# Performance work log

Measured on AMD Instinct MI355X. Metric: run time of the kernel, lower is better.

Reference implementation:

```python
import jax, jax.numpy as jnp
import numpy as np

DIM = 512
HEADS = 16
WIN = (2, 7, 7)
N = WIN[0] * WIN[1] * WIN[2]  # 98
TABLE = (2 * WIN[0] - 1) * (2 * WIN[1] - 1) * (2 * WIN[2] - 1)  # 507


def _rel_pos_index():
    cd, ch, cw = np.arange(WIN[0]), np.arange(WIN[1]), np.arange(WIN[2])
    coords = np.stack(np.meshgrid(cd, ch, cw, indexing='ij'))  # (3, D, H, W)
    flat = coords.reshape(3, -1)  # (3, N)
    rel = flat[:, :, None] - flat[:, None, :]  # (3, N, N)
    rel = rel.transpose(1, 2, 0).copy()
    rel[:, :, 0] += WIN[0] - 1
    rel[:, :, 1] += WIN[1] - 1
    rel[:, :, 2] += WIN[2] - 1
    rel[:, :, 0] *= (2 * WIN[1] - 1) * (2 * WIN[2] - 1)
    rel[:, :, 1] *= 2 * WIN[2] - 1
    return jnp.asarray(rel.sum(-1), dtype=jnp.int32)  # (N, N)


def setup_inputs() -> dict:
    key = jax.random.key(0)
    ks = jax.random.split(key, 7)
    B_ = 1024
    nW = 64
    return {
        'x': jax.random.normal(ks[0], (B_, N, DIM), dtype=jnp.float32),
        'mask': jnp.zeros((nW, N, N), dtype=jnp.float32),
        'qkv_w': jax.random.normal(ks[1], (3 * DIM, DIM), dtype=jnp.float32) * 0.02,
        'qkv_b': jnp.zeros((3 * DIM,), dtype=jnp.float32),
        'proj_w': jax.random.normal(ks[2], (DIM, DIM), dtype=jnp.float32) * 0.02,
        'proj_b': jnp.zeros((DIM,), dtype=jnp.float32),
        'bias_table': jax.random.normal(ks[3], (TABLE, HEADS), dtype=jnp.float32) * 0.02,
        'rel_pos_index': _rel_pos_index(),
    }


def reference(x, mask, qkv_w, qkv_b, proj_w, proj_b, bias_table, rel_pos_index):
    B_, n, C = x.shape
    hd = C // HEADS
    scale = hd ** -0.5
    # qkv projection: (B_, N, 3C) -> (3, B_, H, N, hd)
    qkv = (x @ qkv_w.T + qkv_b).reshape(B_, n, 3, HEADS, hd).transpose(2, 0, 3, 1, 4)
    q, k, v = qkv[0], qkv[1], qkv[2]
    attn = jnp.einsum('bhnd,bhmd->bhnm', q * scale, k)  # (B_, H, N, N)
    # gathered relative position bias: (N, N, H) -> (H, N, N)
    bias = bias_table[rel_pos_index.reshape(-1)].reshape(n, n, HEADS).transpose(2, 0, 1)
    attn = attn + bias[None]
    nW = mask.shape[0]
    attn = attn.reshape(B_ // nW, nW, HEADS, n, n) + mask[None, :, None]
    attn = jax.nn.softmax(attn.reshape(B_, HEADS, n, n), axis=-1)
    out = jnp.einsum('bhnm,bhmd->bnhd', attn, v).reshape(B_, n, C)
    return out @ proj_w.T + proj_b
```

## Files before the change

kernel.cpp:

```cpp
#include <hip/hip_runtime.h>
#include <hip/hip_bf16.h>
#include <stdint.h>

#define DIMC 512
#define NTOK 98

typedef float f32x4 __attribute__((ext_vector_type(4)));
typedef short bf16x8 __attribute__((ext_vector_type(8)));
typedef short bf16x4 __attribute__((ext_vector_type(4)));

__device__ inline unsigned short f2bf(float f) {
    union { float f; uint32_t u; } v; v.f = f;
    uint32_t r = v.u + 0x7fffu + ((v.u >> 16) & 1u);
    return (unsigned short)(r >> 16);
}

__device__ inline bf16x8 cvt8(float4 a, float4 b) {
    bf16x8 r;
    r[0] = (short)f2bf(a.x); r[1] = (short)f2bf(a.y);
    r[2] = (short)f2bf(a.z); r[3] = (short)f2bf(a.w);
    r[4] = (short)f2bf(b.x); r[5] = (short)f2bf(b.y);
    r[6] = (short)f2bf(b.z); r[7] = (short)f2bf(b.w);
    return r;
}

__device__ __forceinline__ void gload16(const void* g, void* l) {
    __builtin_amdgcn_global_load_lds(
        (const __attribute__((address_space(1))) unsigned int*)g,
        (__attribute__((address_space(3))) unsigned int*)l, 16, 0, 0);
}

#define CFENCE() __asm__ __volatile__("" ::: "memory")
#define BARRIER() do { CFENCE(); __builtin_amdgcn_s_barrier(); CFENCE(); } while (0)

__global__ void k_cvt(const float* __restrict__ src, unsigned short* __restrict__ dst,
                      int n8) {
    int i = blockIdx.x * blockDim.x + threadIdx.x;
    if (i < n8) {
        float4 a = *(const float4*)(src + (size_t)i * 8);
        float4 b = *(const float4*)(src + (size_t)i * 8 + 4);
        *(bf16x8*)(dst + (size_t)i * 8) = cvt8(a, b);
    }
}

__global__ void k_bm(const float* __restrict__ table, const int* __restrict__ idx,
                     const float* __restrict__ mask, float* __restrict__ bm_t) {
    int slice = blockIdx.x;
    int b64 = slice >> 4, h = slice & 15;
    float* dst = bm_t + (size_t)slice * 11200;
    const float* mp = mask + (size_t)b64 * 9604;
    for (int t = threadIdx.x; t < 11200; t += blockDim.x) {
        int c = t / 100, i = t - c * 100;
        float v = -1e9f;
        if (c < NTOK && i < NTOK)
            v = (table[idx[i * NTOK + c] * 16 + h] + mp[i * NTOK + c])
                * 1.4426950408889634f;
        dst[t] = v;
    }
}

__global__ __launch_bounds__(512, 2)
void k_qkv3(const unsigned short* __restrict__ xb, const unsigned short* __restrict__ wb,
            const float* __restrict__ qb, unsigned short* __restrict__ qkvbuf) {
    __shared__ unsigned short As[2][2][128 * 64];
    __shared__ unsigned short Bs[2][2][128 * 64];
    const int tid = threadIdx.x;
    const int wid = tid >> 6, l = tid & 63, g = l >> 4, li = l & 15;
    const int wm = wid >> 2, wn = wid & 3;
    const int id = blockIdx.x;
    const int xcd = id & 7, local = id >> 3;
    const int mt = xcd * 49 + local / 6;
    const int nt = local - (local / 6) * 6;
    const int m0 = mt * 256, n0 = nt * 256;

    const int srow = tid >> 3;
    const int scg  = tid & 7;
    const int sxor = (scg ^ (srow & 7)) * 8;
    const unsigned short* aG[2][2];
    const unsigned short* bG[2][2];
    #pragma unroll
    for (int h = 0; h < 2; ++h) {
        aG[h][0] = xb + (size_t)(m0 + h * 128 + srow) * DIMC + sxor;
        aG[h][1] = xb + (size_t)(m0 + h * 128 + 64 + srow) * DIMC + sxor;
        bG[h][0] = wb + (size_t)(n0 + h * 128 + srow) * DIMC + sxor;
        bG[h][1] = wb + (size_t)(n0 + h * 128 + 64 + srow) * DIMC + sxor;
    }
    const int lb0 = wid * 512;
    const int lb1 = 4096 + wid * 512;

    const int axor0 = ((0 + g) ^ (li & 7)) * 8;
    const int axor1 = ((4 + g) ^ (li & 7)) * 8;
    const int arow = li * 64;
    const int brow = (wn & 1) * 4096 + li * 64;
    const int bh = wn >> 1;

    f32x4 acc[8][4] = {};

#define STAGE(s, kt) do {                                   \
        gload16(aG[0][0] + (kt) * 64, &As[s][0][lb0]);      \
        gload16(aG[0][1] + (kt) * 64, &As[s][0][lb1]);      \
        gload16(aG[1][0] + (kt) * 64, &As[s][1][lb0]);      \
        gload16(aG[1][1] + (kt) * 64, &As[s][1][lb1]);      \
        gload16(bG[0][0] + (kt) * 64, &Bs[s][0][lb0]);      \
        gload16(bG[0][1] + (kt) * 64, &Bs[s][0][lb1]);      \
        gload16(bG[1][0] + (kt) * 64, &Bs[s][1][lb0]);      \
        gload16(bG[1][1] + (kt) * 64, &Bs[s][1][lb1]);      } while (0)

    STAGE(0, 0);
    #pragma unroll
    for (int kt = 0; kt < 8; ++kt) {
        const int s = kt & 1;
        if (kt < 7) {
            STAGE(s ^ 1, kt + 1);
            __asm__ __volatile__("s_waitcnt vmcnt(8)" ::: "memory");
        } else {
            __asm__ __volatile__("s_waitcnt vmcnt(0)" ::: "memory");
        }
        BARRIER();
        bf16x8 bfr[4][2];
        #pragma unroll
        for (int nq = 0; nq < 4; ++nq) {
            bfr[nq][0] = *(const bf16x8*)&Bs[s][bh][brow + nq * 1024 + axor0];
            bfr[nq][1] = *(const bf16x8*)&Bs[s][bh][brow + nq * 1024 + axor1];
        }
        #pragma unroll
        for (int q = 0; q < 4; ++q) {
            bf16x8 a00 = *(const bf16x8*)&As[s][wm][arow + (2 * q) * 1024 + axor0];
            bf16x8 a01 = *(const bf16x8*)&As[s][wm][arow + (2 * q) * 1024 + axor1];
            bf16x8 a10 = *(const bf16x8*)&As[s][wm][arow + (2 * q + 1) * 1024 + axor0];
            bf16x8 a11 = *(const bf16x8*)&As[s][wm][arow + (2 * q + 1) * 1024 + axor1];
            __builtin_amdgcn_s_setprio(1);
            #pragma unroll
            for (int nq = 0; nq < 4; ++nq) {
                acc[2 * q][nq] = __builtin_amdgcn_mfma_f32_16x16x32_bf16(
                    bfr[nq][0], a00, acc[2 * q][nq], 0, 0, 0);
                acc[2 * q][nq] = __builtin_amdgcn_mfma_f32_16x16x32_bf16(
                    bfr[nq][1], a01, acc[2 * q][nq], 0, 0, 0);
                acc[2 * q + 1][nq] = __builtin_amdgcn_mfma_f32_16x16x32_bf16(
                    bfr[nq][0], a10, acc[2 * q + 1][nq], 0, 0, 0);
                acc[2 * q + 1][nq] = __builtin_amdgcn_mfma_f32_16x16x32_bf16(
                    bfr[nq][1], a11, acc[2 * q + 1][nq], 0, 0, 0);
            }
            __builtin_amdgcn_s_setprio(0);
        }
        BARRIER();
    }
#undef STAGE

    #pragma unroll
    for (int mq = 0; mq < 8; ++mq) {
        int row = m0 + wm * 128 + mq * 16 + li;
        unsigned bw = (unsigned)row / 98u;
        unsigned nn_ = (unsigned)row - bw * 98u;
        unsigned short* rbase = qkvbuf + (size_t)bw * 150528u + nn_ * 32u;
        #pragma unroll
        for (int nq = 0; nq < 4; ++nq) {
            int col0 = n0 + wn * 64 + nq * 16 + g * 4;
            int which = col0 >> 9;
            int h = (col0 >> 5) & 15;
            int d0 = col0 & 31;
            float4 bv = *(const float4*)(qb + col0);
            float sc = (which == 0)
                ? (0.17677669529663689f * 1.4426950408889634f) : 1.0f;
            bf16x4 pk;
            pk[0] = (short)f2bf((acc[mq][nq][0] + bv.x) * sc);
            pk[1] = (short)f2bf((acc[mq][nq][1] + bv.y) * sc);
            pk[2] = (short)f2bf((acc[mq][nq][2] + bv.z) * sc);
            pk[3] = (short)f2bf((acc[mq][nq][3] + bv.w) * sc);
            *(bf16x4*)(rbase + (size_t)(h * 3 + which) * 3136u + d0) = pk;
        }
    }
}

__global__ __launch_bounds__(512, 2)
void k_proj3(const unsigned short* __restrict__ qkvbuf,
             const unsigned short* __restrict__ wb,
             const float* __restrict__ pb, float* __restrict__ out) {
    __shared__ unsigned short As[2][2][128 * 64];
    __shared__ unsigned short Bs[2][2][128 * 64];
    const int tid = threadIdx.x;
    const int wid = tid >> 6, l = tid & 63, g = l >> 4, li = l & 15;
    const int wm = wid >> 2, wn = wid & 3;
    const int id = blockIdx.x;
    const int xcd = id & 7, local = id >> 3;
    const int mt = xcd * 49 + local / 2;
    const int nt = local & 1;
    const int m0 = mt * 256, n0 = nt * 256;

    const int srow = tid >> 3;
    const int scg  = tid & 7;
    const int cgx  = scg ^ (srow & 7);
    const unsigned short* aG[2][2];
    const unsigned short* bG[2][2];
    #pragma unroll
    for (int h = 0; h < 2; ++h) {
        #pragma unroll
        for (int i = 0; i < 2; ++i) {
            int R = m0 + h * 128 + i * 64 + srow;
            unsigned bw = (unsigned)R / 98u, nn = (unsigned)R - bw * 98u;
            aG[h][i] = qkvbuf + (size_t)bw * 150528u + nn * 32u
                       + (size_t)(cgx >> 2) * 9408u + (cgx & 3) * 8;
            bG[h][i] = wb + (size_t)(n0 + h * 128 + i * 64 + srow) * DIMC + cgx * 8;
        }
    }
    const int lb0 = wid * 512;
    const int lb1 = 4096 + wid * 512;

    const int axor0 = ((0 + g) ^ (li & 7)) * 8;
    const int axor1 = ((4 + g) ^ (li & 7)) * 8;
    const int arow = li * 64;
    const int brow = (wn & 1) * 4096 + li * 64;
    const int bh = wn >> 1;

    f32x4 acc[8][4] = {};

#define STAGE(s, kt) do {                                               \
        gload16(aG[0][0] + (size_t)(kt) * 18816u, &As[s][0][lb0]);      \
        gload16(aG[0][1] + (size_t)(kt) * 18816u, &As[s][0][lb1]);      \
        gload16(aG[1][0] + (size_t)(kt) * 18816u, &As[s][1][lb0]);      \
        gload16(aG[1][1] + (size_t)(kt) * 18816u, &As[s][1][lb1]);      \
        gload16(bG[0][0] + (kt) * 64, &Bs[s][0][lb0]);                  \
        gload16(bG[0][1] + (kt) * 64, &Bs[s][0][lb1]);                  \
        gload16(bG[1][0] + (kt) * 64, &Bs[s][1][lb0]);                  \
        gload16(bG[1][1] + (kt) * 64, &Bs[s][1][lb1]);                  } while (0)

    STAGE(0, 0);
    #pragma unroll
    for (int kt = 0; kt < 8; ++kt) {
        const int s = kt & 1;
        if (kt < 7) {
            STAGE(s ^ 1, kt + 1);
            __asm__ __volatile__("s_waitcnt vmcnt(8)" ::: "memory");
        } else {
            __asm__ __volatile__("s_waitcnt vmcnt(0)" ::: "memory");
        }
        BARRIER();
        bf16x8 bfr[4][2];
        #pragma unroll
        for (int nq = 0; nq < 4; ++nq) {
            bfr[nq][0] = *(const bf16x8*)&Bs[s][bh][brow + nq * 1024 + axor0];
            bfr[nq][1] = *(const bf16x8*)&Bs[s][bh][brow + nq * 1024 + axor1];
        }
        #pragma unroll
        for (int q = 0; q < 4; ++q) {
            bf16x8 a00 = *(const bf16x8*)&As[s][wm][arow + (2 * q) * 1024 + axor0];
            bf16x8 a01 = *(const bf16x8*)&As[s][wm][arow + (2 * q) * 1024 + axor1];
            bf16x8 a10 = *(const bf16x8*)&As[s][wm][arow + (2 * q + 1) * 1024 + axor0];
            bf16x8 a11 = *(const bf16x8*)&As[s][wm][arow + (2 * q + 1) * 1024 + axor1];
            __builtin_amdgcn_s_setprio(1);
            #pragma unroll
            for (int nq = 0; nq < 4; ++nq) {
                acc[2 * q][nq] = __builtin_amdgcn_mfma_f32_16x16x32_bf16(
                    bfr[nq][0], a00, acc[2 * q][nq], 0, 0, 0);
                acc[2 * q][nq] = __builtin_amdgcn_mfma_f32_16x16x32_bf16(
                    bfr[nq][1], a01, acc[2 * q][nq], 0, 0, 0);
                acc[2 * q + 1][nq] = __builtin_amdgcn_mfma_f32_16x16x32_bf16(
                    bfr[nq][0], a10, acc[2 * q + 1][nq], 0, 0, 0);
                acc[2 * q + 1][nq] = __builtin_amdgcn_mfma_f32_16x16x32_bf16(
                    bfr[nq][1], a11, acc[2 * q + 1][nq], 0, 0, 0);
            }
            __builtin_amdgcn_s_setprio(0);
        }
        BARRIER();
    }
#undef STAGE

    #pragma unroll
    for (int mq = 0; mq < 8; ++mq) {
        int row2 = m0 + wm * 128 + mq * 16 + li;
        float* orow = out + (size_t)row2 * DIMC;
        #pragma unroll
        for (int nq = 0; nq < 4; ++nq) {
            int col0 = n0 + wn * 64 + nq * 16 + g * 4;
            float4 bv = *(const float4*)(pb + col0);
            float4 v;
            v.x = acc[mq][nq][0] + bv.x;
            v.y = acc[mq][nq][1] + bv.y;
            v.z = acc[mq][nq][2] + bv.z;
            v.w = acc[mq][nq][3] + bv.w;
            *(float4*)(orow + col0) = v;
        }
    }
}

__global__ __launch_bounds__(448)
void k_attn(unsigned short* __restrict__ qkvbuf, const float* __restrict__ bm_t) {
    __shared__ short Ks[112][36];
    __shared__ short Vt[32][132];
    __shared__ short Ps[7][16][132];

    const int tid = threadIdx.x;
    const int w = tid >> 6, l = tid & 63, g = l >> 4, li = l & 15;
    const int bh = blockIdx.x;
    const int slice = bh & 1023;

    unsigned short* qslot = qkvbuf + (size_t)bh * 3 * 3136;
    const unsigned short* kslot = qslot + 3136;
    const unsigned short* vslot = qslot + 6272;

    const float* bmp = bm_t + (size_t)slice * 11200 + (16 * w + g * 4);
    f32x4 bmf[7];
    #pragma unroll
    for (int j = 0; j < 7; ++j)
        bmf[j] = *(const f32x4*)(bmp + (16 * j + li) * 100);

    bf16x8 aq = *(const bf16x8*)(qslot + (16 * w + li) * 32 + g * 8);

    if (tid < 392) {
        int row = tid >> 2, seg = (tid & 3) * 8;
        bf16x8 kv = *(const bf16x8*)(kslot + row * 32 + seg);
        *(bf16x8*)&Ks[row][seg] = kv;
        bf16x8 vv = *(const bf16x8*)(vslot + row * 32 + seg);
        #pragma unroll
        for (int j = 0; j < 8; ++j) Vt[seg + j][row] = vv[j];
    }
    Ks[98 + (tid >> 5)][tid & 31] = 0;
    for (int t2 = tid; t2 < 32 * 34; t2 += 448) {
        int d = t2 / 34, c = t2 % 34;
        Vt[d][98 + c] = 0;
    }
    for (int t2 = l; t2 < 16 * 20; t2 += 64) {
        int r = t2 / 20, c = t2 % 20;
        Ps[w][r][112 + c] = 0;
    }

    __syncthreads();

    f32x4 s[7];
    __builtin_amdgcn_s_setprio(1);
    #pragma unroll
    for (int j = 0; j < 7; ++j) {
        bf16x8 bk = *(bf16x8*)&Ks[16 * j + li][g * 8];
        s[j] = __builtin_amdgcn_mfma_f32_16x16x32_bf16(aq, bk, bmf[j], 0, 0, 0);
    }
    __builtin_amdgcn_s_setprio(0);

    float sinv[4];
    #pragma unroll
    for (int r = 0; r < 4; ++r) {
        float mx = s[0][r];
        #pragma unroll
        for (int j = 1; j < 7; ++j) mx = fmaxf(mx, s[j][r]);
        mx = fmaxf(mx, __shfl_xor(mx, 1));
        mx = fmaxf(mx, __shfl_xor(mx, 2));
        mx = fmaxf(mx, __shfl_xor(mx, 4));
        mx = fmaxf(mx, __shfl_xor(mx, 8));
        float sum = 0.f;
        #pragma unroll
        for (int j = 0; j < 7; ++j) {
            float p = exp2f(s[j][r] - mx);
            sum += p;
            Ps[w][g * 4 + r][16 * j + li] = (short)f2bf(p);
        }
        sum += __shfl_xor(sum, 1);
        sum += __shfl_xor(sum, 2);
        sum += __shfl_xor(sum, 4);
        sum += __shfl_xor(sum, 8);
        sinv[r] = 1.0f / sum;
    }

    __syncthreads();

    f32x4 o[2] = {};
    __builtin_amdgcn_s_setprio(1);
    #pragma unroll
    for (int ks = 0; ks < 4; ++ks) {
        bf16x8 pa = *(bf16x8*)&Ps[w][li][ks * 32 + g * 8];
        #pragma unroll
        for (int ct = 0; ct < 2; ++ct) {
            bf16x8 vb = *(bf16x8*)&Vt[ct * 16 + li][ks * 32 + g * 8];
            o[ct] = __builtin_amdgcn_mfma_f32_16x16x32_bf16(pa, vb, o[ct], 0, 0, 0);
        }
    }
    __builtin_amdgcn_s_setprio(0);

    #pragma unroll
    for (int ct = 0; ct < 2; ++ct) {
        #pragma unroll
        for (int r = 0; r < 4; ++r) {
            int i = 16 * w + g * 4 + r;
            if (i < NTOK) {
                int d = ct * 16 + li;
                qslot[i * 32 + d] = f2bf(o[ct][r] * sinv[r]);
            }
        }
    }
}

__global__ void k_bias(const float* __restrict__ table, const int* __restrict__ idx,
                       float* __restrict__ bias_full) {
    int h = blockIdx.x, i = blockIdx.y, j = threadIdx.x;
    if (j < NTOK)
        bias_full[(h * NTOK + i) * NTOK + j] = table[idx[i * NTOK + j] * 16 + h];
}

__global__ __launch_bounds__(256)
void k_qkv_old(const float* __restrict__ x, const float* __restrict__ w,
               const float* __restrict__ qb, unsigned short* __restrict__ qkvbuf) {
    __shared__ short As[128][36];
    __shared__ short Bs[128][36];
    const int tid = threadIdx.x;
    const int m0 = blockIdx.x * 128, n0 = blockIdx.y * 128;
    const int wid = tid >> 6, l = tid & 63;
    const int wr = wid >> 1, wc = wid & 1;
    const int g = l >> 4, li = l & 15;
    const int srow = tid >> 1, scol = (tid & 1) * 16;

    f32x4 acc[4][4] = {};
    const float* ap = x + (size_t)(m0 + srow) * DIMC + scol;
    const float* bp = w + (size_t)(n0 + srow) * DIMC + scol;

    for (int k0 = 0; k0 < DIMC; k0 += 32) {
        float4 a0 = *(const float4*)(ap + k0);
        float4 a1 = *(const float4*)(ap + k0 + 4);
        float4 a2 = *(const float4*)(ap + k0 + 8);
        float4 a3 = *(const float4*)(ap + k0 + 12);
        float4 b0 = *(const float4*)(bp + k0);
        float4 b1 = *(const float4*)(bp + k0 + 4);
        float4 b2 = *(const float4*)(bp + k0 + 8);
        float4 b3 = *(const float4*)(bp + k0 + 12);
        *(bf16x8*)&As[srow][scol]     = cvt8(a0, a1);
        *(bf16x8*)&As[srow][scol + 8] = cvt8(a2, a3);
        *(bf16x8*)&Bs[srow][scol]     = cvt8(b0, b1);
        *(bf16x8*)&Bs[srow][scol + 8] = cvt8(b2, b3);
        __syncthreads();
        bf16x8 af[4], bfr[4];
        #pragma unroll
        for (int mm = 0; mm < 4; ++mm)
            af[mm] = *(bf16x8*)&As[wr * 64 + mm * 16 + li][g * 8];
        #pragma unroll
        for (int nn = 0; nn < 4; ++nn)
            bfr[nn] = *(bf16x8*)&Bs[wc * 64 + nn * 16 + li][g * 8];
        #pragma unroll
        for (int mm = 0; mm < 4; ++mm)
            #pragma unroll
            for (int nn = 0; nn < 4; ++nn)
                acc[mm][nn] = __builtin_amdgcn_mfma_f32_16x16x32_bf16(
                    af[mm], bfr[nn], acc[mm][nn], 0, 0, 0);
        __syncthreads();
    }

    #pragma unroll
    for (int mm = 0; mm < 4; ++mm) {
        #pragma unroll
        for (int nn = 0; nn < 4; ++nn) {
            int col = n0 + wc * 64 + nn * 16 + li;
            int which = col >> 9;
            int h = (col >> 5) & 15;
            int d = col & 31;
            float bv = qb[col];
            #pragma unroll
            for (int r = 0; r < 4; ++r) {
                int row = m0 + wr * 64 + mm * 16 + g * 4 + r;
                unsigned bw = (unsigned)row / 98u;
                unsigned nn_ = (unsigned)row - bw * 98u;
                float v = acc[mm][nn][r] + bv;
                if (which == 0) v *= 0.17677669529663689f;
                qkvbuf[(size_t)((bw * 16u + h) * 3u + which) * 3136u + nn_ * 32u + d] =
                    f2bf(v);
            }
        }
    }
}

__global__ __launch_bounds__(448)
void k_attn_old(unsigned short* __restrict__ qkvbuf, const float* __restrict__ mask,
                const float* __restrict__ bias_full) {
    __shared__ short Ks[112][36];
    __shared__ short Vt[32][132];
    __shared__ short Ps[7][16][132];

    const int tid = threadIdx.x;
    const int w = tid >> 6, l = tid & 63, g = l >> 4, li = l & 15;
    const int bh = blockIdx.x;
    const int b = bh >> 4, h = bh & 15;

    unsigned short* qslot = qkvbuf + (size_t)bh * 3 * 3136;
    const unsigned short* kslot = qslot + 3136;
    const unsigned short* vslot = qslot + 6272;

    if (tid < 392) {
        int row = tid >> 2, seg = (tid & 3) * 8;
        bf16x8 kv = *(const bf16x8*)(kslot + row * 32 + seg);
        *(bf16x8*)&Ks[row][seg] = kv;
        bf16x8 vv = *(const bf16x8*)(vslot + row * 32 + seg);
        #pragma unroll
        for (int j = 0; j < 8; ++j) Vt[seg + j][row] = vv[j];
    }
    Ks[98 + (tid >> 5)][tid & 31] = 0;
    for (int t2 = tid; t2 < 32 * 34; t2 += 448) {
        int d = t2 / 34, c = t2 % 34;
        Vt[d][98 + c] = 0;
    }
    for (int t2 = l; t2 < 16 * 20; t2 += 64) {
        int r = t2 / 20, c = t2 % 20;
        Ps[w][r][112 + c] = 0;
    }

    bf16x8 aq = *(const bf16x8*)(qslot + (16 * w + li) * 32 + g * 8);

    __syncthreads();

    f32x4 s[7];
    #pragma unroll
    for (int j = 0; j < 7; ++j) {
        bf16x8 bk = *(bf16x8*)&Ks[16 * j + li][g * 8];
        f32x4 z = {};
        s[j] = __builtin_amdgcn_mfma_f32_16x16x32_bf16(aq, bk, z, 0, 0, 0);
    }

    const float* bp = bias_full + h * 9604;
    const float* mp = mask + (b & 63) * 9604;
    float sinv[4];
    #pragma unroll
    for (int r = 0; r < 4; ++r) {
        int i = 16 * w + g * 4 + r;
        bool rowok = (i < NTOK);
        float sv[7];
        float mx = -1e30f;
        #pragma unroll
        for (int j = 0; j < 7; ++j) {
            int col = 16 * j + li;
            float t = s[j][r];
            if (rowok && col < NTOK) t += bp[i * NTOK + col] + mp[i * NTOK + col];
            else t = -1e30f;
            sv[j] = t;
            mx = fmaxf(mx, t);
        }
        mx = fmaxf(mx, __shfl_xor(mx, 1));
        mx = fmaxf(mx, __shfl_xor(mx, 2));
        mx = fmaxf(mx, __shfl_xor(mx, 4));
        mx = fmaxf(mx, __shfl_xor(mx, 8));
        float sum = 0.f;
        #pragma unroll
        for (int j = 0; j < 7; ++j) {
            float p = __expf(sv[j] - mx);
            sum += p;
            Ps[w][g * 4 + r][16 * j + li] = (short)f2bf(p);
        }
        sum += __shfl_xor(sum, 1);
        sum += __shfl_xor(sum, 2);
        sum += __shfl_xor(sum, 4);
        sum += __shfl_xor(sum, 8);
        sinv[r] = 1.0f / sum;
    }

    __syncthreads();

    f32x4 o[2] = {};
    #pragma unroll
    for (int ks = 0; ks < 4; ++ks) {
        bf16x8 pa = *(bf16x8*)&Ps[w][li][ks * 32 + g * 8];
        #pragma unroll
        for (int ct = 0; ct < 2; ++ct) {
            bf16x8 vb = *(bf16x8*)&Vt[ct * 16 + li][ks * 32 + g * 8];
            o[ct] = __builtin_amdgcn_mfma_f32_16x16x32_bf16(pa, vb, o[ct], 0, 0, 0);
        }
    }

    #pragma unroll
    for (int ct = 0; ct < 2; ++ct) {
        #pragma unroll
        for (int r = 0; r < 4; ++r) {
            int i = 16 * w + g * 4 + r;
            if (i < NTOK) {
                int d = ct * 16 + li;
                qslot[i * 32 + d] = f2bf(o[ct][r] * sinv[r]);
            }
        }
    }
}

__global__ __launch_bounds__(256)
void k_proj_old(const unsigned short* __restrict__ qkvbuf, const float* __restrict__ w,
                const float* __restrict__ pb, float* __restrict__ out) {
    __shared__ short As[128][36];
    __shared__ short Bs[128][36];
    const int tid = threadIdx.x;
    const int m0 = blockIdx.x * 128, n0 = blockIdx.y * 128;
    const int wid = tid >> 6, l = tid & 63;
    const int wr = wid >> 1, wc = wid & 1;
    const int g = l >> 4, li = l & 15;
    const int srow = tid >> 1, scol = (tid & 1) * 16;

    unsigned row = m0 + srow;
    unsigned bw = row / 98u, nn_ = row - bw * 98u;
    const unsigned short* abase =
        qkvbuf + (size_t)bw * 48u * 3136u + (size_t)nn_ * 32u + scol;
    const float* bp = w + (size_t)(n0 + srow) * DIMC + scol;

    f32x4 acc[4][4] = {};

    for (int k0 = 0; k0 < DIMC; k0 += 32) {
        int hh = k0 >> 5;
        const unsigned short* ap = abase + (size_t)hh * 9408u;
        bf16x8 A0 = *(const bf16x8*)ap;
        bf16x8 A1 = *(const bf16x8*)(ap + 8);
        float4 b0 = *(const float4*)(bp + k0);
        float4 b1 = *(const float4*)(bp + k0 + 4);
        float4 b2 = *(const float4*)(bp + k0 + 8);
        float4 b3 = *(const float4*)(bp + k0 + 12);
        *(bf16x8*)&As[srow][scol]     = A0;
        *(bf16x8*)&As[srow][scol + 8] = A1;
        *(bf16x8*)&Bs[srow][scol]     = cvt8(b0, b1);
        *(bf16x8*)&Bs[srow][scol + 8] = cvt8(b2, b3);
        __syncthreads();
        bf16x8 af[4], bfr[4];
        #pragma unroll
        for (int mm = 0; mm < 4; ++mm)
            af[mm] = *(bf16x8*)&As[wr * 64 + mm * 16 + li][g * 8];
        #pragma unroll
        for (int nn = 0; nn < 4; ++nn)
            bfr[nn] = *(bf16x8*)&Bs[wc * 64 + nn * 16 + li][g * 8];
        #pragma unroll
        for (int mm = 0; mm < 4; ++mm)
            #pragma unroll
            for (int nn = 0; nn < 4; ++nn)
                acc[mm][nn] = __builtin_amdgcn_mfma_f32_16x16x32_bf16(
                    af[mm], bfr[nn], acc[mm][nn], 0, 0, 0);
        __syncthreads();
    }

    #pragma unroll
    for (int mm = 0; mm < 4; ++mm) {
        #pragma unroll
        for (int nn = 0; nn < 4; ++nn) {
            int col = n0 + wc * 64 + nn * 16 + li;
            float bv = pb[col];
            #pragma unroll
            for (int r = 0; r < 4; ++r) {
                int row2 = m0 + wr * 64 + mm * 16 + g * 4 + r;
                out[(size_t)row2 * DIMC + col] = acc[mm][nn][r] + bv;
            }
        }
    }
}

extern "C" void kernel_launch(void* const* d_in, const int* in_sizes, int n_in,
                              void* d_out, int out_size, void* d_ws, size_t ws_size,
                              hipStream_t stream) {
    const float* x          = (const float*)d_in[0];
    const float* mask       = (const float*)d_in[1];
    const float* qkv_w      = (const float*)d_in[2];
    const float* qkv_b      = (const float*)d_in[3];
    const float* proj_w     = (const float*)d_in[4];
    const float* proj_b     = (const float*)d_in[5];
    const float* bias_table = (const float*)d_in[6];
    const int*   rel_idx    = (const int*)d_in[7];
    float* out = (float*)d_out;

    const size_t QKV_BYTES = (size_t)16384 * 3 * 3136 * 2;
    const size_t XB_BYTES  = (size_t)100352 * 512 * 2;
    const size_t WQ_BYTES  = (size_t)1536 * 512 * 2;
    const size_t WP_BYTES  = (size_t)512 * 512 * 2;

    unsigned short* qkvbuf = (unsigned short*)d_ws;
    const size_t need = QKV_BYTES + XB_BYTES + WQ_BYTES + WP_BYTES;

    if (ws_size >= need) {
        unsigned short* xb  = (unsigned short*)((char*)d_ws + QKV_BYTES);
        unsigned short* wqb = xb + (size_t)100352 * 512;
        unsigned short* wpb = wqb + (size_t)1536 * 512;
        float* bm_t = (float*)xb;

        k_cvt<<<dim3(25088), dim3(256), 0, stream>>>(x, xb, 6422528);
        k_cvt<<<dim3(384),   dim3(256), 0, stream>>>(qkv_w, wqb, 98304);
        k_cvt<<<dim3(128),   dim3(256), 0, stream>>>(proj_w, wpb, 32768);

        k_qkv3<<<dim3(2352), dim3(512), 0, stream>>>(xb, wqb, qkv_b, qkvbuf);
        k_bm<<<dim3(1024), dim3(256), 0, stream>>>(bias_table, rel_idx, mask, bm_t);
        k_attn<<<dim3(16384), dim3(448), 0, stream>>>(qkvbuf, bm_t);
        k_proj3<<<dim3(784), dim3(512), 0, stream>>>(qkvbuf, wpb, proj_b, out);
    } else {
        float* bias_full = (float*)((char*)d_ws + QKV_BYTES);
        k_bias<<<dim3(16, 98), dim3(128), 0, stream>>>(bias_table, rel_idx, bias_full);
        k_qkv_old<<<dim3(784, 12), dim3(256), 0, stream>>>(x, qkv_w, qkv_b, qkvbuf);
        k_attn_old<<<dim3(16384), dim3(448), 0, stream>>>(qkvbuf, mask, bias_full);
        k_proj_old<<<dim3(784, 4), dim3(256), 0, stream>>>(qkvbuf, proj_w, proj_b, out);
    }
}
```

Measured before the change: 665.3 us.

## Make attention kernel persistent over 8 heads with register-prefetched Q/K/V

The attention kernel now launches 2048 blocks, each looping over 8 head slices that share the same window slice. The bias+mask tile is loaded into registers once per block, and the next head's Q, K and V are prefetched into registers while the current one computes. This amortizes the per-block bias/mask load and launch overhead and hides global load latency. In exchange there are fewer blocks for load balancing, two barriers per iteration, and higher register pressure.

```diff
diff --git a/kernel.cpp b/kernel.cpp
--- a/kernel.cpp
+++ b/kernel.cpp
@@ -284,19 +284,16 @@
 }
 
 __global__ __launch_bounds__(448)
-void k_attn(unsigned short* __restrict__ qkvbuf, const float* __restrict__ bm_t) {
+void k_attn2(unsigned short* __restrict__ qkvbuf, const float* __restrict__ bm_t) {
     __shared__ short Ks[112][36];
     __shared__ short Vt[32][132];
     __shared__ short Ps[7][16][132];
 
     const int tid = threadIdx.x;
     const int w = tid >> 6, l = tid & 63, g = l >> 4, li = l & 15;
-    const int bh = blockIdx.x;
-    const int slice = bh & 1023;
-
-    unsigned short* qslot = qkvbuf + (size_t)bh * 3 * 3136;
-    const unsigned short* kslot = qslot + 3136;
-    const unsigned short* vslot = qslot + 6272;
+
+    const int id = blockIdx.x;
+    const int slice = id >> 1, mh = id & 1;
 
     const float* bmp = bm_t + (size_t)slice * 11200 + (16 * w + g * 4);
     f32x4 bmf[7];
@@ -304,16 +301,6 @@
     for (int j = 0; j < 7; ++j)
         bmf[j] = *(const f32x4*)(bmp + (16 * j + li) * 100);
 
-    bf16x8 aq = *(const bf16x8*)(qslot + (16 * w + li) * 32 + g * 8);
-
-    if (tid < 392) {
-        int row = tid >> 2, seg = (tid & 3) * 8;
-        bf16x8 kv = *(const bf16x8*)(kslot + row * 32 + seg);
-        *(bf16x8*)&Ks[row][seg] = kv;
-        bf16x8 vv = *(const bf16x8*)(vslot + row * 32 + seg);
-        #pragma unroll
-        for (int j = 0; j < 8; ++j) Vt[seg + j][row] = vv[j];
-    }
     Ks[98 + (tid >> 5)][tid & 31] = 0;
     for (int t2 = tid; t2 < 32 * 34; t2 += 448) {
         int d = t2 / 34, c = t2 % 34;
@@ -324,66 +311,97 @@
         Ps[w][r][112 + c] = 0;
     }
 
-    __syncthreads();
-
-    f32x4 s[7];
-    __builtin_amdgcn_s_setprio(1);
-    #pragma unroll
-    for (int j = 0; j < 7; ++j) {
-        bf16x8 bk = *(bf16x8*)&Ks[16 * j + li][g * 8];
-        s[j] = __builtin_amdgcn_mfma_f32_16x16x32_bf16(aq, bk, bmf[j], 0, 0, 0);
-    }
-    __builtin_amdgcn_s_setprio(0);
-
-    float sinv[4];
-    #pragma unroll
-    for (int r = 0; r < 4; ++r) {
-        float mx = s[0][r];
-        #pragma unroll
-        for (int j = 1; j < 7; ++j) mx = fmaxf(mx, s[j][r]);
-        mx = fmaxf(mx, __shfl_xor(mx, 1));
-        mx = fmaxf(mx, __shfl_xor(mx, 2));
-        mx = fmaxf(mx, __shfl_xor(mx, 4));
-        mx = fmaxf(mx, __shfl_xor(mx, 8));
-        float sum = 0.f;
+    const int krow = tid >> 2, kseg = (tid & 3) * 8;
+    const size_t step = (size_t)1024 * 9408;
+    unsigned short* qslot = qkvbuf + (size_t)(mh * 8192 + slice) * 9408;
+
+    bf16x8 kcur = {}, vcur = {}, aqc, knxt = {}, vnxt = {}, aqn;
+    if (tid < 392) {
+        kcur = *(const bf16x8*)(qslot + 3136 + krow * 32 + kseg);
+        vcur = *(const bf16x8*)(qslot + 6272 + krow * 32 + kseg);
+    }
+    aqc = *(const bf16x8*)(qslot + (16 * w + li) * 32 + g * 8);
+
+    for (int it = 0; it < 8; ++it) {
+        if (tid < 392) {
+            *(bf16x8*)&Ks[krow][kseg] = kcur;
+            #pragma unroll
+            for (int j = 0; j < 8; ++j) Vt[kseg + j][krow] = vcur[j];
+        }
+        unsigned short* qnext = qslot + step;
+        if (it < 7) {
+            if (tid < 392) {
+                knxt = *(const bf16x8*)(qnext + 3136 + krow * 32 + kseg);
+                vnxt = *(const bf16x8*)(qnext + 6272 + krow * 32 + kseg);
+            }
+            aqn = *(const bf16x8*)(qnext + (16 * w + li) * 32 + g * 8);
+        }
+        __syncthreads();
+
+        f32x4 s[7];
+        __builtin_amdgcn_s_setprio(1);
         #pragma unroll
         for (int j = 0; j < 7; ++j) {
-            float p = exp2f(s[j][r] - mx);
-            sum += p;
-            Ps[w][g * 4 + r][16 * j + li] = (short)f2bf(p);
-        }
-        sum += __shfl_xor(sum, 1);
-        sum += __shfl_xor(sum, 2);
-        sum += __shfl_xor(sum, 4);
-        sum += __shfl_xor(sum, 8);
-        sinv[r] = 1.0f / sum;
-    }
-
-    __syncthreads();
-
-    f32x4 o[2] = {};
-    __builtin_amdgcn_s_setprio(1);
-    #pragma unroll
-    for (int ks = 0; ks < 4; ++ks) {
-        bf16x8 pa = *(bf16x8*)&Ps[w][li][ks * 32 + g * 8];
+            bf16x8 bk = *(bf16x8*)&Ks[16 * j + li][g * 8];
+            s[j] = __builtin_amdgcn_mfma_f32_16x16x32_bf16(aqc, bk, bmf[j], 0, 0, 0);
+        }
+        __builtin_amdgcn_s_setprio(0);
+
+        float sinv[4];
+        #pragma unroll
+        for (int r = 0; r < 4; ++r) {
+            float mx = s[0][r];
+            #pragma unroll
+            for (int j = 1; j < 7; ++j) mx = fmaxf(mx, s[j][r]);
+            mx = fmaxf(mx, __shfl_xor(mx, 1));
+            mx = fmaxf(mx, __shfl_xor(mx, 2));
+            mx = fmaxf(mx, __shfl_xor(mx, 4));
+            mx = fmaxf(mx, __shfl_xor(mx, 8));
+            float sum = 0.f;
+            #pragma unroll
+            for (int j = 0; j < 7; ++j) {
+                float p = exp2f(s[j][r] - mx);
+                sum += p;
+                Ps[w][g * 4 + r][16 * j + li] = (short)f2bf(p);
+            }
+            sum += __shfl_xor(sum, 1);
+            sum += __shfl_xor(sum, 2);
+            sum += __shfl_xor(sum, 4);
+            sum += __shfl_xor(sum, 8);
+            sinv[r] = 1.0f / sum;
+        }
+
+        __asm__ __volatile__("s_waitcnt lgkmcnt(0)" ::: "memory");
+        __builtin_amdgcn_sched_barrier(0);
+
+        f32x4 o[2] = {};
+        __builtin_amdgcn_s_setprio(1);
+        #pragma unroll
+        for (int ks = 0; ks < 4; ++ks) {
+            bf16x8 pa = *(bf16x8*)&Ps[w][li][ks * 32 + g * 8];
+            #pragma unroll
+            for (int ct = 0; ct < 2; ++ct) {
+                bf16x8 vb = *(bf16x8*)&Vt[ct * 16 + li][ks * 32 + g * 8];
+                o[ct] = __builtin_amdgcn_mfma_f32_16x16x32_bf16(pa, vb, o[ct], 0, 0, 0);
+            }
+        }
+        __builtin_amdgcn_s_setprio(0);
+
         #pragma unroll
         for (int ct = 0; ct < 2; ++ct) {
-            bf16x8 vb = *(bf16x8*)&Vt[ct * 16 + li][ks * 32 + g * 8];
-            o[ct] = __builtin_amdgcn_mfma_f32_16x16x32_bf16(pa, vb, o[ct], 0, 0, 0);
-        }
-    }
-    __builtin_amdgcn_s_setprio(0);
-
-    #pragma unroll
-    for (int ct = 0; ct < 2; ++ct) {
-        #pragma unroll
-        for (int r = 0; r < 4; ++r) {
-            int i = 16 * w + g * 4 + r;
-            if (i < NTOK) {
-                int d = ct * 16 + li;
-                qslot[i * 32 + d] = f2bf(o[ct][r] * sinv[r]);
-            }
-        }
+            #pragma unroll
+            for (int r = 0; r < 4; ++r) {
+                int i = 16 * w + g * 4 + r;
+                if (i < NTOK) {
+                    int d = ct * 16 + li;
+                    qslot[i * 32 + d] = f2bf(o[ct][r] * sinv[r]);
+                }
+            }
+        }
+
+        __syncthreads();
+        kcur = knxt; vcur = vnxt; aqc = aqn;
+        qslot = qnext;
     }
 }
 
@@ -669,7 +687,7 @@
 
         k_qkv3<<<dim3(2352), dim3(512), 0, stream>>>(xb, wqb, qkv_b, qkvbuf);
         k_bm<<<dim3(1024), dim3(256), 0, stream>>>(bias_table, rel_idx, mask, bm_t);
-        k_attn<<<dim3(16384), dim3(448), 0, stream>>>(qkvbuf, bm_t);
+        k_attn2<<<dim3(2048), dim3(448), 0, stream>>>(qkvbuf, bm_t);
         k_proj3<<<dim3(784), dim3(512), 0, stream>>>(qkvbuf, wpb, proj_b, out);
     } else {
         float* bias_full = (float*)((char*)d_ws + QKV_BYTES);
```

After: 647.1 us. -2.7%, faster.
